# Kernel tuning notes

Measured on AMD Instinct MI355X. Metric: run time of the kernel, lower is better.

Reference implementation:

```python
import jax, jax.numpy as jnp
import numpy as np

N_NODES = 40000
N_EDGES = 400000
N_GRAPHS = 256
F_IN = 128
COND = 100
HEADS = 32
DIMS = [90, 45, 15, 5]
EPS = 1e-5


def setup_inputs() -> dict:
    key = jax.random.key(0)
    ks = iter(jax.random.split(key, 64))
    inp = {}
    inp["x"] = jax.random.normal(next(ks), (N_NODES, F_IN), dtype=jnp.float32)
    inp["edge_index"] = jax.random.randint(next(ks), (2, N_EDGES), 0, N_NODES, dtype=jnp.int32)
    inp["batch"] = jnp.sort(jax.random.randint(next(ks), (N_NODES,), 0, N_GRAPHS, dtype=jnp.int32))
    inp["conditional_features"] = jax.random.normal(next(ks), (COND,), dtype=jnp.float32)
    # GATConv params: W [in, H*C], a_src/a_dst [H, C], bias [C] (concat=False -> out is C)
    dims_in = [F_IN] + DIMS[:-1]
    for i, (ci, co) in enumerate(zip(dims_in, DIMS), start=1):
        sw = 1.0 / np.sqrt(ci)
        inp[f"W{i}"] = jax.random.normal(next(ks), (ci, HEADS * co), dtype=jnp.float32) * sw
        inp[f"as{i}"] = jax.random.normal(next(ks), (HEADS, co), dtype=jnp.float32) * (1.0 / np.sqrt(co))
        inp[f"ad{i}"] = jax.random.normal(next(ks), (HEADS, co), dtype=jnp.float32) * (1.0 / np.sqrt(co))
        inp[f"b{i}"] = jnp.zeros((co,), dtype=jnp.float32)
    # BatchNorm affine params (init gamma=1, beta=0) for sizes F_IN,90,45,15,5
    for i, c in enumerate([F_IN] + DIMS, start=1):
        inp[f"g{i}"] = jnp.ones((c,), dtype=jnp.float32)
        inp[f"be{i}"] = jnp.zeros((c,), dtype=jnp.float32)
    inp["fcW"] = jax.random.normal(next(ks), (DIMS[-1] + COND, 1), dtype=jnp.float32) * (1.0 / np.sqrt(DIMS[-1] + COND))
    inp["fcb"] = jnp.zeros((1,), dtype=jnp.float32)
    return inp


def _bn(x, g, b):
    # training-mode BatchNorm1d: batch statistics (biased var), eps=1e-5
    mu = x.mean(0)
    var = x.var(0)
    return g * (x - mu) * jax.lax.rsqrt(var + EPS) + b


def _gat(x, W, a_s, a_d, b, src, dst, n):
    H, C = a_s.shape
    h = (x @ W).reshape(n, H, C)                      # [N,H,C]
    s_src = jnp.einsum("nhc,hc->nh", h, a_s)
    s_dst = jnp.einsum("nhc,hc->nh", h, a_d)
    logit = jax.nn.leaky_relu(s_src[src] + s_dst[dst], 0.2)  # [E,H]
    m = jax.ops.segment_max(logit, dst, num_segments=n)
    e = jnp.exp(logit - m[dst])
    denom = jax.ops.segment_sum(e, dst, num_segments=n)
    alpha = e / denom[dst]                            # per-dst softmax, [E,H]
    out = jnp.zeros((n, C), dtype=x.dtype)
    for hi in range(H):  # fixed small loop over heads keeps peak memory at [E,C]
        out = out + jax.ops.segment_sum(alpha[:, hi, None] * h[src, hi, :], dst, num_segments=n)
    return out / H + b   # concat=False -> mean over heads, then bias


def reference(x, edge_index, batch, conditional_features,
              W1, as1, ad1, b1, W2, as2, ad2, b2, W3, as3, ad3, b3, W4, as4, ad4, b4,
              g1, be1, g2, be2, g3, be3, g4, be4, g5, be5, fcW, fcb):
    n = x.shape[0]
    loop = jnp.arange(n, dtype=edge_index.dtype)      # PyG GATConv adds self-loops by default
    src = jnp.concatenate([edge_index[0], loop])
    dst = jnp.concatenate([edge_index[1], loop])

    h = _bn(x, g1, be1)
    h = jax.nn.leaky_relu(_gat(h, W1, as1, ad1, b1, src, dst, n), 0.01)
    h = _bn(h, g2, be2)
    h = jax.nn.leaky_relu(_gat(h, W2, as2, ad2, b2, src, dst, n), 0.01)
    h = _bn(h, g3, be3)
    h = jax.nn.leaky_relu(_gat(h, W3, as3, ad3, b3, src, dst, n), 0.01)
    h = _bn(h, g4, be4)
    h = jax.nn.leaky_relu(_gat(h, W4, as4, ad4, b4, src, dst, n), 0.01)
    # dropout is identity in eval mode

    counts = jax.ops.segment_sum(jnp.ones((n,), dtype=h.dtype), batch, num_segments=N_GRAPHS)
    pooled = jax.ops.segment_sum(h, batch, num_segments=N_GRAPHS) / jnp.maximum(counts, 1.0)[:, None]
    z = jnp.concatenate([pooled, jnp.broadcast_to(conditional_features, (N_GRAPHS, COND))], axis=1)
    return jax.nn.sigmoid(z @ fcW + fcb).reshape(-1, 1)
```

## Files before the change

### kernel.cpp

```cpp
#include <hip/hip_runtime.h>
#include <hip/hip_bf16.h>

constexpr int NN = 40000;
constexpr int NE = 400000;
constexpr int NSLAB = 20000;
constexpr int MPAD = 20096;
constexpr int MPADX = 40192;
constexpr int SCB = 256;
constexpr int SCHUNK = (NN + SCB - 1) / SCB;
constexpr int NPB = 512;

__device__ __forceinline__ unsigned short f2bf(float f) {
    unsigned int u = __float_as_uint(f);
    unsigned int r = (u + 0x7FFFu + ((u >> 16) & 1u)) >> 16;
    return (unsigned short)r;
}

__device__ __forceinline__ unsigned int cvt_pk_bf16(float a, float b) {
    unsigned int r;
    asm("v_cvt_pk_bf16_f32 %0, %1, %2" : "=v"(r) : "v"(a), "v"(b));
    return r;
}

__device__ __forceinline__ void load_lds16(const unsigned short* g, unsigned short* l) {
    __builtin_amdgcn_global_load_lds(
        (const __attribute__((address_space(1))) unsigned int*)(g),
        (__attribute__((address_space(3))) unsigned int*)(l), 16, 0, 0);
}

typedef __attribute__((ext_vector_type(8))) short bf16x8;
typedef __attribute__((ext_vector_type(4))) float f32x4;
typedef __attribute__((ext_vector_type(2))) float floatx2;

__global__ void bn_partial(const float* __restrict__ x, int N, int C,
                           float* __restrict__ partial) {
    int ch = threadIdx.x;
    if (ch >= C) return;
    float s = 0.f, sq = 0.f;
    for (int n = blockIdx.x; n < N; n += gridDim.x) {
        float v = x[(size_t)n * C + ch];
        s += v; sq += v * v;
    }
    partial[(size_t)blockIdx.x * 2 * C + ch]     = s;
    partial[(size_t)blockIdx.x * 2 * C + C + ch] = sq;
}

template <int CIN, int CP, int NB>
__global__ __launch_bounds__(256) void bn_apply_f(const float* __restrict__ x,
                                                  const float* __restrict__ partial,
                                                  const float* __restrict__ g,
                                                  const float* __restrict__ be,
                                                  float* __restrict__ scale_g,
                                                  float* __restrict__ shift_g,
                                                  unsigned short* __restrict__ xbn) {
    __shared__ float hs[2][128], hq[2][128];
    __shared__ float sc_l[CP], sh_l[CP];
    const int tid = threadIdx.x;
    const int half = tid >> 7, ch = tid & 127;
    if (ch < CIN) {
        constexpr int H = NB / 2;
        int b0 = half ? H : 0;
        int b1 = half ? NB : H;
        float s = 0.f, sq = 0.f;
#pragma unroll 8
        for (int b = b0; b < b1; ++b) {
            s  += partial[(size_t)b * 2 * CIN + ch];
            sq += partial[(size_t)b * 2 * CIN + CIN + ch];
        }
        hs[half][ch] = s; hq[half][ch] = sq;
    }
    __syncthreads();
    if (tid < CP) {
        float sc = 0.f, sh = 0.f;
        if (tid < CIN) {
            float s  = hs[0][tid] + hs[1][tid];
            float sq = hq[0][tid] + hq[1][tid];
            float mean = s / (float)NN;
            float var  = sq / (float)NN - mean * mean;
            float inv  = rsqrtf(var + 1e-5f);
            sc = g[tid] * inv;
            sh = be[tid] - mean * sc;
            if (blockIdx.x == 0) { scale_g[tid] = sc; shift_g[tid] = sh; }
        }
        sc_l[tid] = sc; sh_l[tid] = sh;
    }
    __syncthreads();
    const int total = NN * (CP / 2);
    for (int idx = blockIdx.x * 256 + tid; idx < total; idx += 256 * gridDim.x) {
        int n = idx / (CP / 2), c2 = idx % (CP / 2);
        int c = 2 * c2;
        float v0 = 0.f, v1 = 0.f;
        if (c < CIN)     v0 = sc_l[c] * x[(size_t)n * CIN + c] + sh_l[c];
        if (c + 1 < CIN) v1 = sc_l[c + 1] * x[(size_t)n * CIN + c + 1] + sh_l[c + 1];
        reinterpret_cast<unsigned int*>(xbn)[idx] = cvt_pk_bf16(v0, v1);
    }
}

struct PrepLayer {
    const float* W; const float* as_; const float* ad_;
    float* Wf; unsigned short* Wft; unsigned short* Wt;
    int CIN, CP, COUT, NP, bbase;
};
struct PrepArgs { PrepLayer L[4]; int nb; };

__global__ void prep_all(PrepArgs A) {
    int bid = blockIdx.x;
    int li = 0;
#pragma unroll
    for (int i = 1; i < 4; ++i)
        if (bid >= A.L[i].bbase) li = i;
    const PrepLayer& P = A.L[li];
    const int CIN = P.CIN, CP = P.CP, COUT = P.COUT;
    int b = bid - P.bbase;
    int tid = threadIdx.x;
    if (b < CP) {
        int cin = b;
        if (tid < 64) {
            int j = tid, h = j & 31;
            float s = 0.f;
            if (cin < CIN) {
                const float* a = (j < 32) ? P.as_ : P.ad_;
                const float* wrow = P.W + (size_t)cin * 32 * COUT + (size_t)h * COUT;
                const float* arow = a + (size_t)h * COUT;
                for (int c = 0; c < COUT; ++c) s += wrow[c] * arow[c];
            }
            P.Wf[cin * 64 + j] = s;
            P.Wft[j * CP + cin] = f2bf(s);
        }
    } else {
        int c = b - CP;
        for (int kk = tid; kk < 32 * CP; kk += blockDim.x) {
            int h = kk / CP, k = kk % CP;
            float v = 0.f;
            if (k < CIN && c < COUT)
                v = P.W[(size_t)k * (32 * COUT) + h * COUT + c] * (1.f / 32.f);
            P.Wt[(size_t)c * (32 * CP) + kk] = f2bf(v);
        }
    }
}

template <int CPK>
__global__ __launch_bounds__(256) void gemm_s(const unsigned short* __restrict__ xbn,
                                              const unsigned short* __restrict__ Wft,
                                              float* __restrict__ Sbuf) {
    constexpr int NC = CPK / 32;
    __shared__ unsigned short Ab[64 * 32];
    __shared__ unsigned short Bb[64 * 32];
    const int m0 = blockIdx.x * 64;
    const int tid = threadIdx.x;
    const int wv = tid >> 6, lane = tid & 63;
    const int mm = lane & 15, quad = lane >> 4;
    f32x4 acc[4];
#pragma unroll
    for (int t = 0; t < 4; ++t) acc[t] = f32x4{0.f, 0.f, 0.f, 0.f};

    for (int c = 0; c < NC; ++c) {
        int row = tid >> 2, gc = tid & 3;
        load_lds16(xbn + (size_t)(m0 + row) * CPK + c * 32 + gc * 8, Ab + (size_t)tid * 8);
        load_lds16(Wft + (size_t)row * CPK + c * 32 + gc * 8, Bb + (size_t)tid * 8);
        asm volatile("s_waitcnt vmcnt(0)" ::: "memory");
        __syncthreads();
        bf16x8 a = *reinterpret_cast<const bf16x8*>(&Ab[(wv * 16 + mm) * 32 + quad * 8]);
#pragma unroll
        for (int t = 0; t < 4; ++t) {
            bf16x8 b = *reinterpret_cast<const bf16x8*>(&Bb[(t * 16 + mm) * 32 + quad * 8]);
            acc[t] = __builtin_amdgcn_mfma_f32_16x16x32_bf16(a, b, acc[t], 0, 0, 0);
        }
        __syncthreads();
    }
    int rbase = m0 + wv * 16 + quad * 4;
#pragma unroll
    for (int t = 0; t < 4; ++t)
#pragma unroll
        for (int r = 0; r < 4; ++r)
            Sbuf[(size_t)(rbase + r) * 64 + t * 16 + mm] = acc[t][r];
}

__global__ __launch_bounds__(256) void gemm_bn(const float* __restrict__ X,
                                               const float* __restrict__ W,
                                               const float* __restrict__ scale,
                                               const float* __restrict__ shift,
                                               int Cin, int HC, float* __restrict__ OUT) {
    __shared__ float As[8][64];
    __shared__ float Bs[8][64];
    int tid = threadIdx.x;
    int n0 = blockIdx.y * 64;
    int j0 = blockIdx.x * 64;
    int tr = tid >> 4, tc = tid & 15;
    float acc[4][4] = {};
    for (int k0 = 0; k0 < Cin; k0 += 8) {
        int idx = tid;
#pragma unroll
        for (int it = 0; it < 2; ++it, idx += 256) {
            int row = idx >> 3, kk = idx & 7;
            int k = k0 + kk;
            float v = 0.f;
            if (k < Cin) v = scale[k] * X[(size_t)(n0 + row) * Cin + k] + shift[k];
            As[kk][row] = v;
        }
        int idx2 = tid;
#pragma unroll
        for (int it = 0; it < 2; ++it, idx2 += 256) {
            int col = idx2 & 63, kr = idx2 >> 6;
            int k = k0 + kr, j = j0 + col;
            float v = 0.f;
            if (k < Cin && j < HC) v = W[(size_t)k * HC + j];
            Bs[kr][col] = v;
        }
        __syncthreads();
#pragma unroll
        for (int kk = 0; kk < 8; ++kk) {
            float a[4], b[4];
#pragma unroll
            for (int i = 0; i < 4; ++i) a[i] = As[kk][tr * 4 + i];
#pragma unroll
            for (int j = 0; j < 4; ++j) b[j] = Bs[kk][tc * 4 + j];
#pragma unroll
            for (int i = 0; i < 4; ++i)
#pragma unroll
                for (int j = 0; j < 4; ++j) acc[i][j] += a[i] * b[j];
        }
        __syncthreads();
    }
#pragma unroll
    for (int i = 0; i < 4; ++i) {
        int row = n0 + tr * 4 + i;
#pragma unroll
        for (int j = 0; j < 4; ++j) {
            int col = j0 + tc * 4 + j;
            if (col < HC) OUT[(size_t)row * HC + col] = acc[i][j];
        }
    }
}

__global__ void count_kernel(const int* __restrict__ dst, int* __restrict__ deg) {
    int e = blockIdx.x * blockDim.x + threadIdx.x;
    if (e < NE) atomicAdd(&deg[dst[e]], 1);
}
__global__ void scan_pass1(const int* __restrict__ deg, int* __restrict__ bsum) {
    __shared__ int red[256];
    int b = blockIdx.x, t = threadIdx.x;
    int lo = b * SCHUNK, hi = min(lo + SCHUNK, NN);
    int s = 0;
    for (int i = lo + t; i < hi; i += 256) s += deg[i] + 1;
    red[t] = s;
    __syncthreads();
    for (int off = 128; off > 0; off >>= 1) {
        if (t < off) red[t] += red[t + off];
        __syncthreads();
    }
    if (t == 0) bsum[b] = red[0];
}
__global__ void scan_pass2(const int* __restrict__ bsum, int* __restrict__ boff,
                           int* __restrict__ rowptr) {
    __shared__ int lds[256];
    int t = threadIdx.x;
    int v0 = bsum[t];
    lds[t] = v0;
    __syncthreads();
    for (int off = 1; off < 256; off <<= 1) {
        int v = (t >= off) ? lds[t - off] : 0;
        __syncthreads();
        lds[t] += v;
        __syncthreads();
    }
    boff[t] = lds[t] - v0;
    if (t == 255) rowptr[NN] = lds[255];
}
__global__ void scan_pass3(const int* __restrict__ deg, const int* __restrict__ boff,
                           int* __restrict__ rowptr, int* __restrict__ cursor) {
    __shared__ int lds[256];
    int b = blockIdx.x, t = threadIdx.x;
    int i = b * SCHUNK + t;
    int d = (t < SCHUNK && i < NN) ? (deg[i] + 1) : 0;
    lds[t] = d;
    __syncthreads();
    for (int off = 1; off < 256; off <<= 1) {
        int v = (t >= off) ? lds[t - off] : 0;
        __syncthreads();
        lds[t] += v;
        __syncthreads();
    }
    if (t < SCHUNK && i < NN) {
        int excl = lds[t] - d + boff[b];
        rowptr[i] = excl;
        cursor[i] = excl;
    }
}
__global__ void scatter_all(const int* __restrict__ src, const int* __restrict__ dst,
                            int* __restrict__ cursor, int* __restrict__ colsrc) {
    int e = blockIdx.x * blockDim.x + threadIdx.x;
    if (e < NE) {
        int pos = atomicAdd(&cursor[dst[e]], 1);
        colsrc[pos] = src[e];
    } else if (e < NE + NN) {
        int n = e - NE;
        int pos = atomicAdd(&cursor[n], 1);
        colsrc[pos] = n;
    }
}

template <int CIN, int CP>
__global__ __launch_bounds__(256) void agg_x(const unsigned short* __restrict__ xbn,
                                             const float* __restrict__ S,
                                             const int* __restrict__ rowptr,
                                             const int* __restrict__ colsrc,
                                             int n0, unsigned short* __restrict__ z) {
    constexpr int BS = 256, CH = 16, J = CP / 8;
    constexpr bool V4 = (J % 4 == 0);
    constexpr int NACC = V4 ? (J / 4) : (J / 2);
    constexpr int LIT = CH * 32 / 256;
    __shared__ __align__(16) float x_lds[CH * CP];
    __shared__ float w_lds[CH * 32];
    __shared__ int cs_lds[CH];
    __shared__ float red_m[8][32];
    __shared__ float red_s[8][32];

    int n = n0 + blockIdx.x;
    int tid = threadIdx.x;
    int start = rowptr[n], end = rowptr[n + 1];
    const int h = tid & 31, g = tid >> 5;
    const int cbase = g * J;
    const float sd = S[(size_t)n * 64 + 32 + h];

    float m_reg = -INFINITY, d_reg = 0.f;
    f32x4 acc4[V4 ? NACC : 1];
    floatx2 acc2[V4 ? 1 : NACC];
    if constexpr (V4) {
#pragma unroll
        for (int j = 0; j < NACC; ++j) acc4[j] = f32x4{0.f, 0.f, 0.f, 0.f};
    } else {
#pragma unroll
        for (int j = 0; j < NACC; ++j) acc2[j] = floatx2{0.f, 0.f};
    }

    for (int chunk = start; chunk < end; chunk += CH) {
        int ce = min(CH, end - chunk);
        int ce32 = ce * 32;
        if (tid < CH && tid < ce) cs_lds[tid] = colsrc[chunk + tid];
        __syncthreads();

        float lreg[LIT];
        float pmx = -INFINITY;
#pragma unroll
        for (int p = 0; p < LIT; ++p) {
            int idx = p * 256 + tid;
            lreg[p] = -INFINITY;
            if (idx < ce32) {
                int e = idx >> 5;
                float l = S[(size_t)cs_lds[e] * 64 + h] + sd;
                l = l > 0.f ? l : 0.2f * l;
                lreg[p] = l;
                pmx = fmaxf(pmx, l);
            }
        }
        red_m[g][h] = pmx;
        for (int idx = tid; idx < ce * (CP / 4); idx += BS) {
            int e = idx / (CP / 4), c4 = idx % (CP / 4);
            uint2 u = reinterpret_cast<const uint2*>(xbn)[(size_t)cs_lds[e] * (CP / 4) + c4];
            f32x4 t;
            t[0] = __uint_as_float(u.x << 16);
            t[1] = __uint_as_float(u.x & 0xFFFF0000u);
            t[2] = __uint_as_float(u.y << 16);
            t[3] = __uint_as_float(u.y & 0xFFFF0000u);
            *reinterpret_cast<f32x4*>(&x_lds[e * CP + 4 * c4]) = t;
        }
        __syncthreads();

        float cm = red_m[0][h];
#pragma unroll
        for (int s2 = 1; s2 < 8; ++s2) cm = fmaxf(cm, red_m[s2][h]);
        float newm = fmaxf(m_reg, cm);
        float r = (m_reg == -INFINITY) ? 0.f : __expf(m_reg - newm);
        m_reg = newm;

        float ps = 0.f;
#pragma unroll
        for (int p = 0; p < LIT; ++p) {
            int idx = p * 256 + tid;
            if (idx < ce32) {
                float v = __expf(lreg[p] - m_reg);
                w_lds[idx] = v;
                ps += v;
            }
        }
        red_s[g][h] = ps;
        __syncthreads();

        float ss = red_s[0][h];
#pragma unroll
        for (int s2 = 1; s2 < 8; ++s2) ss += red_s[s2][h];
        d_reg = d_reg * r + ss;

        if constexpr (V4) {
            f32x4 rr4 = {r, r, r, r};
#pragma unroll
            for (int j = 0; j < NACC; ++j) acc4[j] *= rr4;
            for (int e = 0; e < ce; ++e) {
                float w = w_lds[e * 32 + h];
                f32x4 w4 = {w, w, w, w};
                const f32x4* xv = reinterpret_cast<const f32x4*>(&x_lds[e * CP + cbase]);
#pragma unroll
                for (int j = 0; j < NACC; ++j) acc4[j] += w4 * xv[j];
            }
        } else {
            floatx2 rr2 = {r, r};
#pragma unroll
            for (int j = 0; j < NACC; ++j) acc2[j] *= rr2;
            for (int e = 0; e < ce; ++e) {
                float w = w_lds[e * 32 + h];
                floatx2 w2 = {w, w};
                const floatx2* xv = reinterpret_cast<const floatx2*>(&x_lds[e * CP + cbase]);
#pragma unroll
                for (int j = 0; j < NACC; ++j) acc2[j] += w2 * xv[j];
            }
        }
    }

    float dinv = 1.f / d_reg;
    if constexpr (V4) {
        uint2* zp = reinterpret_cast<uint2*>(
            z + (size_t)(n - n0) * (32 * CP) + h * CP + cbase);
#pragma unroll
        for (int j = 0; j < NACC; ++j) {
            uint2 t;
            t.x = cvt_pk_bf16(acc4[j][0] * dinv, acc4[j][1] * dinv);
            t.y = cvt_pk_bf16(acc4[j][2] * dinv, acc4[j][3] * dinv);
            zp[j] = t;
        }
    } else {
        unsigned int* zp = reinterpret_cast<unsigned int*>(
            z + (size_t)(n - n0) * (32 * CP) + h * CP + cbase);
#pragma unroll
        for (int j = 0; j < NACC; ++j)
            zp[j] = cvt_pk_bf16(acc2[j][0] * dinv, acc2[j][1] * dinv);
    }
}

template <int NT, int KP, int KS, bool FB, bool STATS>
__global__ __launch_bounds__(256) void gemm_z_t(const unsigned short* __restrict__ z,
                                                const unsigned short* __restrict__ Wt,
                                                float* __restrict__ obuf,
                                                const float* __restrict__ bias,
                                                int n0, int COUT, int nr, int pstride,
                                                float* __restrict__ statp) {
    constexpr int NP = NT * 16;
    constexpr int KSEG = KP / KS;
    constexpr int NC = KSEG / 64;
    constexpr int MT = 64;
    __shared__ unsigned short Abuf[2][MT * 64];
    __shared__ unsigned short Bbuf[2][NP * 64];

    const int m0 = blockIdx.x * MT;
    const int kbeg = blockIdx.y * KSEG;
    const int tid = threadIdx.x;
    const int wv = tid >> 6;
    const int lane = tid & 63;
    const int mm = lane & 15, quad = lane >> 4;

    auto stage = [&](int buf, int kk) {
#pragma unroll
        for (int it = 0; it < 2; ++it) {
            int gi = it * 256 + tid;
            int row = gi >> 3, gc = gi & 7;
            int srow = m0 + row;
            if (srow > nr - 1) srow = nr - 1;
            const unsigned short* src = z + (size_t)srow * KP + kk + gc * 8;
            unsigned short* dst = &Abuf[buf][(size_t)(it * 256 + wv * 64) * 8];
            load_lds16(src, dst);
        }
#pragma unroll
        for (int it = 0; it < (NP * 8 + 255) / 256; ++it) {
            int gi = it * 256 + tid;
            if (gi < NP * 8) {
                int row = gi >> 3, gc = gi & 7;
                const unsigned short* src = Wt + (size_t)row * KP + kk + gc * 8;
                unsigned short* dst = &Bbuf[buf][(size_t)(it * 256 + wv * 64) * 8];
                load_lds16(src, dst);
            }
        }
    };

    f32x4 acc[NT];
#pragma unroll
    for (int t = 0; t < NT; ++t) acc[t] = f32x4{0.f, 0.f, 0.f, 0.f};

    stage(0, kbeg);
    for (int c = 0; c < NC; ++c) {
        asm volatile("s_waitcnt vmcnt(0)" ::: "memory");
        __syncthreads();
        int cur = c & 1;
        if (c + 1 < NC) stage(cur ^ 1, kbeg + (c + 1) * 64);
        const unsigned short* Ab = Abuf[cur];
        const unsigned short* Bb = Bbuf[cur];
#pragma unroll
        for (int hh = 0; hh < 2; ++hh) {
            bf16x8 a0 = *reinterpret_cast<const bf16x8*>(&Ab[(wv * 16 + mm) * 64 + hh * 32 + quad * 8]);
#pragma unroll
            for (int t = 0; t < NT; ++t) {
                bf16x8 b = *reinterpret_cast<const bf16x8*>(&Bb[(t * 16 + mm) * 64 + hh * 32 + quad * 8]);
                acc[t] = __builtin_amdgcn_mfma_f32_16x16x32_bf16(a0, b, acc[t], 0, 0, 0);
            }
        }
        __syncthreads();
    }

    int row0 = quad * 4;
    if constexpr (FB) {
        float s = 0.f, q = 0.f;
#pragma unroll
        for (int t = 0; t < NT; ++t) {
            int cc = t * 16 + mm;
#pragma unroll
            for (int r = 0; r < 4; ++r) {
                int m = m0 + wv * 16 + row0 + r;
                if (m < nr && cc < COUT) {
                    float v = acc[t][r] + bias[cc];
                    v = v > 0.f ? v : 0.01f * v;
                    obuf[(size_t)(n0 + m) * COUT + cc] = v;
                    if constexpr (STATS) { s += v; q += v * v; }
                }
            }
        }
        if constexpr (STATS) {
            static_assert(NT == 1, "STATS path assumes NT==1");
            __shared__ float ssum[4][4][16], sqsum[4][4][16];
            ssum[wv][quad][mm] = s; sqsum[wv][quad][mm] = q;
            __syncthreads();
            if (tid < 16) {
                float S = 0.f, Q = 0.f;
#pragma unroll
                for (int a = 0; a < 4; ++a)
#pragma unroll
                    for (int b2 = 0; b2 < 4; ++b2) {
                        S += ssum[a][b2][tid]; Q += sqsum[a][b2][tid];
                    }
                if (tid < COUT) {
                    statp[(size_t)blockIdx.x * 2 * COUT + tid] = S;
                    statp[(size_t)blockIdx.x * 2 * COUT + COUT + tid] = Q;
                }
            }
        }
    } else {
        float* pb = obuf + (size_t)blockIdx.y * pstride * NP;
#pragma unroll
        for (int t = 0; t < NT; ++t) {
            int cc = t * 16 + mm;
#pragma unroll
            for (int r = 0; r < 4; ++r) {
                int m = m0 + wv * 16 + row0 + r;
                pb[(size_t)m * NP + cc] = acc[t][r];
            }
        }
    }
}

__global__ void reduce_parts(const float* __restrict__ pbuf, int KS, int NPAD, int COUT,
                             const float* __restrict__ bias, int n0, int nr, int pstride,
                             float* __restrict__ xout) {
    int idx = blockIdx.x * blockDim.x + threadIdx.x;
    if (idx >= nr * NPAD) return;
    int m = idx / NPAD, c = idx % NPAD;
    if (c >= COUT) return;
    float s = 0.f;
    for (int p = 0; p < KS; ++p) s += pbuf[(size_t)p * pstride * NPAD + (size_t)m * NPAD + c];
    float v = s + bias[c];
    v = v > 0.f ? v : 0.01f * v;
    xout[(size_t)(n0 + m) * COUT + c] = v;
}

__global__ __launch_bounds__(64) void pool_head(const float* __restrict__ x4,
                                                const int* __restrict__ batch,
                                                const float* __restrict__ cond,
                                                const float* __restrict__ fcW,
                                                const float* __restrict__ fcb,
                                                float* __restrict__ out) {
    int g = blockIdx.x;
    int lane = threadIdx.x;
    int lo = 0, hi = NN;
    while (lo < hi) { int mid = (lo + hi) >> 1; if (batch[mid] < g) lo = mid + 1; else hi = mid; }
    int lo2 = lo, hi2 = NN;
    while (lo2 < hi2) { int mid = (lo2 + hi2) >> 1; if (batch[mid] < g + 1) lo2 = mid + 1; else hi2 = mid; }
    int beg = lo, end = lo2;

    float s[5] = {0.f, 0.f, 0.f, 0.f, 0.f};
    for (int n = beg + lane; n < end; n += 64) {
#pragma unroll
        for (int c = 0; c < 5; ++c) s[c] += x4[(size_t)n * 5 + c];
    }
    float cz = 0.f;
    if (lane < 100) cz = cond[lane] * fcW[5 + lane];
    if (lane + 64 < 100) cz += cond[lane + 64] * fcW[5 + lane + 64];
#pragma unroll
    for (int off = 32; off > 0; off >>= 1) {
#pragma unroll
        for (int c = 0; c < 5; ++c) s[c] += __shfl_down(s[c], off, 64);
        cz += __shfl_down(cz, off, 64);
    }
    if (lane == 0) {
        float cnt = fmaxf((float)(end - beg), 1.f);
        float zv = fcb[0] + cz;
#pragma unroll
        for (int c = 0; c < 5; ++c) zv += (s[c] / cnt) * fcW[c];
        out[g] = 1.f / (1.f + __expf(-zv));
    }
}

struct LayerBufs {
    float* scale; float* shift;
    unsigned short* xbn; unsigned short* zbuf;
    float* Sbuf; float* pbuf; const int* rowptr; const int* colsrc;
};

template <int CIN, int CP, int COUT, int NP, int NT, int KS, int SLABS, int NB, bool OSTATS>
static void run_layer(const float* xin, const float* sp_in,
                      const float* Wf, const unsigned short* Wft,
                      const unsigned short* Wt,
                      const float* Bv, const float* G, const float* Be,
                      float* xout, float* statp, int pstride,
                      const LayerBufs& B, hipStream_t stream) {
    constexpr int KP = 32 * CP;
    constexpr int NPAD = NT * 16;
    constexpr int NR = NN / SLABS;
    constexpr int NTILE = (NR + 63) / 64;
    bn_apply_f<CIN, CP, NB><<<512, 256, 0, stream>>>(xin, sp_in, G, Be,
                                                     B.scale, B.shift, B.xbn);
    if constexpr (CP >= 64) {
        gemm_s<CP><<<NN / 64, 256, 0, stream>>>(B.xbn, Wft, B.Sbuf);
    } else {
        gemm_bn<<<dim3(1, NN / 64), 256, 0, stream>>>(xin, Wf, B.scale, B.shift, CIN, 64, B.Sbuf);
    }
    for (int s = 0; s < SLABS; ++s) {
        int n0 = s * NR;
        agg_x<CIN, CP><<<NR, 256, 0, stream>>>(B.xbn, B.Sbuf, B.rowptr, B.colsrc, n0, B.zbuf);
        if constexpr (KS > 1) {
            gemm_z_t<NT, KP, KS, false, false><<<dim3(NTILE, KS), 256, 0, stream>>>(
                B.zbuf, Wt, B.pbuf, nullptr, n0, COUT, NR, pstride, nullptr);
            reduce_parts<<<((size_t)NR * NPAD + 255) / 256, 256, 0, stream>>>(
                B.pbuf, KS, NPAD, COUT, Bv, n0, NR, pstride, xout);
        } else {
            gemm_z_t<NT, KP, 1, true, OSTATS><<<dim3(NTILE, 1), 256, 0, stream>>>(
                B.zbuf, Wt, xout, Bv, n0, COUT, NR, pstride, statp);
        }
    }
}

extern "C" void kernel_launch(void* const* d_in, const int* in_sizes, int n_in,
                              void* d_out, int out_size, void* d_ws, size_t ws_size,
                              hipStream_t stream) {
    (void)in_sizes; (void)n_in; (void)out_size;
    const float* x     = (const float*)d_in[0];
    const int*   ei    = (const int*)d_in[1];
    const int*   batch = (const int*)d_in[2];
    const float* cond  = (const float*)d_in[3];
    const float* W[4]  = {(const float*)d_in[4],  (const float*)d_in[8],
                          (const float*)d_in[12], (const float*)d_in[16]};
    const float* Asp[4] = {(const float*)d_in[5],  (const float*)d_in[9],
                           (const float*)d_in[13], (const float*)d_in[17]};
    const float* Adp[4] = {(const float*)d_in[6],  (const float*)d_in[10],
                           (const float*)d_in[14], (const float*)d_in[18]};
    const float* Bv[4]  = {(const float*)d_in[7],  (const float*)d_in[11],
                           (const float*)d_in[15], (const float*)d_in[19]};
    const float* G[4]   = {(const float*)d_in[20], (const float*)d_in[22],
                           (const float*)d_in[24], (const float*)d_in[26]};
    const float* Be[4]  = {(const float*)d_in[21], (const float*)d_in[23],
                           (const float*)d_in[25], (const float*)d_in[27]};
    const float* fcW = (const float*)d_in[30];
    const float* fcb = (const float*)d_in[31];
    float* out = (float*)d_out;

    const int CPs[4]  = {128, 96, 48, 16};
    const int NPs[4]  = {96, 48, 16, 16};
    const int CINs[4] = {128, 90, 45, 15};
    const int COUTs[4] = {90, 45, 15, 5};

    auto layout_total = [&](size_t zb, size_t pb) -> size_t {
        size_t o = 0;
        auto a = [&](size_t b) { o += (b + 255) & ~(size_t)255; };
        a(zb); a((size_t)NN * 128 * 2); a(pb); a((size_t)NN * 90 * 4);
        a((size_t)NN * 64 * 4); a((size_t)NPB * 2 * 128 * 4); a((size_t)NPB * 2 * 128 * 4);
        a(128 * 4); a(128 * 4);
        for (int i = 0; i < 4; ++i) {
            a((size_t)CPs[i] * 64 * 4); a((size_t)64 * CPs[i] * 2);
            a((size_t)NPs[i] * 32 * CPs[i] * 2);
        }
        a((size_t)NN * 4); a((size_t)(NN + 1) * 4); a((size_t)NN * 4);
        a((size_t)(NE + NN) * 4); a((size_t)SCB * 4); a((size_t)SCB * 4);
        return o;
    };
    const size_t zb_big = (size_t)NN * 4096 * 2, pb_big = (size_t)4 * MPADX * 96 * 4;
    const size_t zb_sm  = (size_t)NSLAB * 4096 * 2, pb_sm = (size_t)4 * MPAD * 96 * 4;
    const bool big = layout_total(zb_big, pb_big) <= ws_size;
    const size_t zb = big ? zb_big : zb_sm;
    const size_t pbb = big ? pb_big : pb_sm;
    const int pstride = big ? MPADX : MPAD;

    char* base = (char*)d_ws;
    size_t off = 0;
    auto alloc = [&](size_t b) {
        size_t o = off;
        off += (b + 255) & ~(size_t)255;
        return (void*)(base + o);
    };
    unsigned short* zbuf = (unsigned short*)alloc(zb);
    unsigned short* xbn  = (unsigned short*)alloc((size_t)NN * 128 * 2);
    float* pbuf    = (float*)alloc(pbb);
    float* xbuf    = (float*)alloc((size_t)NN * 90 * 4);
    float* Sbuf    = (float*)alloc((size_t)NN * 64 * 4);
    float* partial = (float*)alloc((size_t)NPB * 2 * 128 * 4);
    float* stat1   = (float*)alloc((size_t)NPB * 2 * 128 * 4);
    float* scale   = (float*)alloc(128 * 4);
    float* shift   = (float*)alloc(128 * 4);
    float* Wf_a[4]; unsigned short* Wft_a[4]; unsigned short* Wt_a[4];
    for (int i = 0; i < 4; ++i) {
        Wf_a[i]  = (float*)alloc((size_t)CPs[i] * 64 * 4);
        Wft_a[i] = (unsigned short*)alloc((size_t)64 * CPs[i] * 2);
        Wt_a[i]  = (unsigned short*)alloc((size_t)NPs[i] * 32 * CPs[i] * 2);
    }
    int* deg     = (int*)alloc((size_t)NN * 4);
    int* rowptr  = (int*)alloc((size_t)(NN + 1) * 4);
    int* cursor  = (int*)alloc((size_t)NN * 4);
    int* colsrc  = (int*)alloc((size_t)(NE + NN) * 4);
    int* bsum    = (int*)alloc((size_t)SCB * 4);
    int* boff    = (int*)alloc((size_t)SCB * 4);
    if (off > ws_size) return;

    const int* srcp = ei;
    const int* dstp = ei + NE;

    PrepArgs PA;
    int bb = 0;
    for (int i = 0; i < 4; ++i) {
        PA.L[i] = PrepLayer{W[i], Asp[i], Adp[i], Wf_a[i], Wft_a[i], Wt_a[i],
                            CINs[i], CPs[i], COUTs[i], NPs[i], bb};
        bb += CPs[i] + NPs[i];
    }
    PA.nb = bb;
    prep_all<<<bb, 256, 0, stream>>>(PA);

    hipMemsetAsync(deg, 0, (size_t)NN * 4, stream);
    count_kernel<<<(NE + 255) / 256, 256, 0, stream>>>(dstp, deg);
    scan_pass1<<<SCB, 256, 0, stream>>>(deg, bsum);
    scan_pass2<<<1, 256, 0, stream>>>(bsum, boff, rowptr);
    scan_pass3<<<SCB, 256, 0, stream>>>(deg, boff, rowptr, cursor);
    scatter_all<<<(NE + NN + 255) / 256, 256, 0, stream>>>(srcp, dstp, cursor, colsrc);

    LayerBufs B{scale, shift, xbn, zbuf, Sbuf, pbuf, rowptr, colsrc};

    if (big) {
        bn_partial<<<NPB, 128, 0, stream>>>(x, NN, 128, partial);
        run_layer<128, 128, 90, 96, 6, 4, 1, NPB, false>(x, partial,
            Wf_a[0], Wft_a[0], Wt_a[0], Bv[0], G[0], Be[0], xbuf, nullptr, pstride, B, stream);
        bn_partial<<<NPB, 128, 0, stream>>>(xbuf, NN, 90, partial);
        run_layer< 90,  96, 45, 48, 3, 3, 1, NPB, false>(xbuf, partial,
            Wf_a[1], Wft_a[1], Wt_a[1], Bv[1], G[1], Be[1], xbuf, nullptr, pstride, B, stream);
        bn_partial<<<NPB, 128, 0, stream>>>(xbuf, NN, 45, partial);
        run_layer< 45,  48, 15, 16, 1, 1, 1, NPB, true >(xbuf, partial,
            Wf_a[2], Wft_a[2], Wt_a[2], Bv[2], G[2], Be[2], xbuf, stat1, pstride, B, stream);
        run_layer< 15,  16,  5, 16, 1, 1, 1, 625, false>(xbuf, stat1,
            Wf_a[3], Wft_a[3], Wt_a[3], Bv[3], G[3], Be[3], xbuf, nullptr, pstride, B, stream);
    } else {
        bn_partial<<<NPB, 128, 0, stream>>>(x, NN, 128, partial);
        run_layer<128, 128, 90, 96, 6, 4, 2, NPB, false>(x, partial,
            Wf_a[0], Wft_a[0], Wt_a[0], Bv[0], G[0], Be[0], xbuf, nullptr, pstride, B, stream);
        bn_partial<<<NPB, 128, 0, stream>>>(xbuf, NN, 90, partial);
        run_layer< 90,  96, 45, 48, 3, 3, 2, NPB, false>(xbuf, partial,
            Wf_a[1], Wft_a[1], Wt_a[1], Bv[1], G[1], Be[1], xbuf, nullptr, pstride, B, stream);
        bn_partial<<<NPB, 128, 0, stream>>>(xbuf, NN, 45, partial);
        run_layer< 45,  48, 15, 16, 1, 1, 1, NPB, true >(xbuf, partial,
            Wf_a[2], Wft_a[2], Wt_a[2], Bv[2], G[2], Be[2], xbuf, stat1, pstride, B, stream);
        run_layer< 15,  16,  5, 16, 1, 1, 1, 625, false>(xbuf, stat1,
            Wf_a[3], Wft_a[3], Wt_a[3], Bv[3], G[3], Be[3], xbuf, nullptr, pstride, B, stream);
    }

    pool_head<<<256, 64, 0, stream>>>(xbuf, batch, cond, fcW, fcb, out);
}
```

Measured before the change: 951.0 us.

## Use f32x4 accumulators in agg_x for small widths and add mid workspace mode

```diff
diff --git a/kernel.cpp b/kernel.cpp
--- a/kernel.cpp
+++ b/kernel.cpp
@@ -30,7 +30,6 @@
 
 typedef __attribute__((ext_vector_type(8))) short bf16x8;
 typedef __attribute__((ext_vector_type(4))) float f32x4;
-typedef __attribute__((ext_vector_type(2))) float floatx2;
 
 __global__ void bn_partial(const float* __restrict__ x, int N, int C,
                            float* __restrict__ partial) {
@@ -306,9 +305,10 @@
                                              const int* __restrict__ rowptr,
                                              const int* __restrict__ colsrc,
                                              int n0, unsigned short* __restrict__ z) {
-    constexpr int BS = 256, CH = 16, J = CP / 8;
-    constexpr bool V4 = (J % 4 == 0);
-    constexpr int NACC = V4 ? (J / 4) : (J / 2);
+    constexpr int BS = 256, CH = 16;
+    constexpr int J = (CP >= 64) ? (CP / 8) : 8;
+    constexpr int NG = CP / J;
+    constexpr int NACC = J / 4;
     constexpr int LIT = CH * 32 / 256;
     __shared__ __align__(16) float x_lds[CH * CP];
     __shared__ float w_lds[CH * 32];
@@ -321,18 +321,13 @@
     int start = rowptr[n], end = rowptr[n + 1];
     const int h = tid & 31, g = tid >> 5;
     const int cbase = g * J;
+    const bool act = (g < NG);
     const float sd = S[(size_t)n * 64 + 32 + h];
 
     float m_reg = -INFINITY, d_reg = 0.f;
-    f32x4 acc4[V4 ? NACC : 1];
-    floatx2 acc2[V4 ? 1 : NACC];
-    if constexpr (V4) {
-#pragma unroll
-        for (int j = 0; j < NACC; ++j) acc4[j] = f32x4{0.f, 0.f, 0.f, 0.f};
-    } else {
-#pragma unroll
-        for (int j = 0; j < NACC; ++j) acc2[j] = floatx2{0.f, 0.f};
-    }
+    f32x4 acc4[NACC];
+#pragma unroll
+    for (int j = 0; j < NACC; ++j) acc4[j] = f32x4{0.f, 0.f, 0.f, 0.f};
 
     for (int chunk = start; chunk < end; chunk += CH) {
         int ce = min(CH, end - chunk);
@@ -392,7 +387,7 @@
         for (int s2 = 1; s2 < 8; ++s2) ss += red_s[s2][h];
         d_reg = d_reg * r + ss;
 
-        if constexpr (V4) {
+        if (act) {
             f32x4 rr4 = {r, r, r, r};
 #pragma unroll
             for (int j = 0; j < NACC; ++j) acc4[j] *= rr4;
@@ -403,22 +398,11 @@
 #pragma unroll
                 for (int j = 0; j < NACC; ++j) acc4[j] += w4 * xv[j];
             }
-        } else {
-            floatx2 rr2 = {r, r};
-#pragma unroll
-            for (int j = 0; j < NACC; ++j) acc2[j] *= rr2;
-            for (int e = 0; e < ce; ++e) {
-                float w = w_lds[e * 32 + h];
-                floatx2 w2 = {w, w};
-                const floatx2* xv = reinterpret_cast<const floatx2*>(&x_lds[e * CP + cbase]);
-#pragma unroll
-                for (int j = 0; j < NACC; ++j) acc2[j] += w2 * xv[j];
-            }
-        }
-    }
-
-    float dinv = 1.f / d_reg;
-    if constexpr (V4) {
+        }
+    }
+
+    if (act) {
+        float dinv = 1.f / d_reg;
         uint2* zp = reinterpret_cast<uint2*>(
             z + (size_t)(n - n0) * (32 * CP) + h * CP + cbase);
 #pragma unroll
@@ -428,12 +412,6 @@
             t.y = cvt_pk_bf16(acc4[j][2] * dinv, acc4[j][3] * dinv);
             zp[j] = t;
         }
-    } else {
-        unsigned int* zp = reinterpret_cast<unsigned int*>(
-            z + (size_t)(n - n0) * (32 * CP) + h * CP + cbase);
-#pragma unroll
-        for (int j = 0; j < NACC; ++j)
-            zp[j] = cvt_pk_bf16(acc2[j][0] * dinv, acc2[j][1] * dinv);
     }
 }
 
@@ -689,11 +667,14 @@
         return o;
     };
     const size_t zb_big = (size_t)NN * 4096 * 2, pb_big = (size_t)4 * MPADX * 96 * 4;
+    const size_t zb_mid = (size_t)NN * 3072 * 2;
+    const size_t pb_mid = (size_t)4 * MPAD * 96 * 4;
     const size_t zb_sm  = (size_t)NSLAB * 4096 * 2, pb_sm = (size_t)4 * MPAD * 96 * 4;
-    const bool big = layout_total(zb_big, pb_big) <= ws_size;
-    const size_t zb = big ? zb_big : zb_sm;
-    const size_t pbb = big ? pb_big : pb_sm;
-    const int pstride = big ? MPADX : MPAD;
+    int mode = 2;
+    if (layout_total(zb_big, pb_big) <= ws_size) mode = 0;
+    else if (layout_total(zb_mid, pb_mid) <= ws_size) mode = 1;
+    const size_t zb = (mode == 0) ? zb_big : (mode == 1) ? zb_mid : zb_sm;
+    const size_t pbb = (mode == 0) ? pb_big : (mode == 1) ? pb_mid : pb_sm;
 
     char* base = (char*)d_ws;
     size_t off = 0;
@@ -747,31 +728,31 @@
 
     LayerBufs B{scale, shift, xbn, zbuf, Sbuf, pbuf, rowptr, colsrc};
 
-    if (big) {
-        bn_partial<<<NPB, 128, 0, stream>>>(x, NN, 128, partial);
+    bn_partial<<<NPB, 128, 0, stream>>>(x, NN, 128, partial);
+    if (mode == 0) {
         run_layer<128, 128, 90, 96, 6, 4, 1, NPB, false>(x, partial,
-            Wf_a[0], Wft_a[0], Wt_a[0], Bv[0], G[0], Be[0], xbuf, nullptr, pstride, B, stream);
+            Wf_a[0], Wft_a[0], Wt_a[0], Bv[0], G[0], Be[0], xbuf, nullptr, MPADX, B, stream);
         bn_partial<<<NPB, 128, 0, stream>>>(xbuf, NN, 90, partial);
         run_layer< 90,  96, 45, 48, 3, 3, 1, NPB, false>(xbuf, partial,
-            Wf_a[1], Wft_a[1], Wt_a[1], Bv[1], G[1], Be[1], xbuf, nullptr, pstride, B, stream);
-        bn_partial<<<NPB, 128, 0, stream>>>(xbuf, NN, 45, partial);
-        run_layer< 45,  48, 15, 16, 1, 1, 1, NPB, true >(xbuf, partial,
-            Wf_a[2], Wft_a[2], Wt_a[2], Bv[2], G[2], Be[2], xbuf, stat1, pstride, B, stream);
-        run_layer< 15,  16,  5, 16, 1, 1, 1, 625, false>(xbuf, stat1,
-            Wf_a[3], Wft_a[3], Wt_a[3], Bv[3], G[3], Be[3], xbuf, nullptr, pstride, B, stream);
+            Wf_a[1], Wft_a[1], Wt_a[1], Bv[1], G[1], Be[1], xbuf, nullptr, MPADX, B, stream);
+    } else if (mode == 1) {
+        run_layer<128, 128, 90, 96, 6, 4, 2, NPB, false>(x, partial,
+            Wf_a[0], Wft_a[0], Wt_a[0], Bv[0], G[0], Be[0], xbuf, nullptr, MPAD, B, stream);
+        bn_partial<<<NPB, 128, 0, stream>>>(xbuf, NN, 90, partial);
+        run_layer< 90,  96, 45, 48, 3, 3, 1, NPB, false>(xbuf, partial,
+            Wf_a[1], Wft_a[1], Wt_a[1], Bv[1], G[1], Be[1], xbuf, nullptr, MPADX, B, stream);
     } else {
-        bn_partial<<<NPB, 128, 0, stream>>>(x, NN, 128, partial);
         run_layer<128, 128, 90, 96, 6, 4, 2, NPB, false>(x, partial,
-            Wf_a[0], Wft_a[0], Wt_a[0], Bv[0], G[0], Be[0], xbuf, nullptr, pstride, B, stream);
+            Wf_a[0], Wft_a[0], Wt_a[0], Bv[0], G[0], Be[0], xbuf, nullptr, MPAD, B, stream);
         bn_partial<<<NPB, 128, 0, stream>>>(xbuf, NN, 90, partial);
         run_layer< 90,  96, 45, 48, 3, 3, 2, NPB, false>(xbuf, partial,
-            Wf_a[1], Wft_a[1], Wt_a[1], Bv[1], G[1], Be[1], xbuf, nullptr, pstride, B, stream);
-        bn_partial<<<NPB, 128, 0, stream>>>(xbuf, NN, 45, partial);
-        run_layer< 45,  48, 15, 16, 1, 1, 1, NPB, true >(xbuf, partial,
-            Wf_a[2], Wft_a[2], Wt_a[2], Bv[2], G[2], Be[2], xbuf, stat1, pstride, B, stream);
-        run_layer< 15,  16,  5, 16, 1, 1, 1, 625, false>(xbuf, stat1,
-            Wf_a[3], Wft_a[3], Wt_a[3], Bv[3], G[3], Be[3], xbuf, nullptr, pstride, B, stream);
-    }
+            Wf_a[1], Wft_a[1], Wt_a[1], Bv[1], G[1], Be[1], xbuf, nullptr, MPAD, B, stream);
+    }
+    bn_partial<<<NPB, 128, 0, stream>>>(xbuf, NN, 45, partial);
+    run_layer< 45,  48, 15, 16, 1, 1, 1, NPB, true >(xbuf, partial,
+        Wf_a[2], Wft_a[2], Wt_a[2], Bv[2], G[2], Be[2], xbuf, stat1, MPADX, B, stream);
+    run_layer< 15,  16,  5, 16, 1, 1, 1, 625, false>(xbuf, stat1,
+        Wf_a[3], Wft_a[3], Wt_a[3], Bv[3], G[3], Be[3], xbuf, nullptr, MPADX, B, stream);
 
     pool_head<<<256, 64, 0, stream>>>(xbuf, batch, cond, fcW, fcb, out);
 }
```

New measurement: 937.8 us. No clear change (-1.4%).
